# Optimization experiments

Measured on AMD Instinct MI355X. Metric: run time of the kernel, lower is better.

The kernel has to match this reference:

```python
import jax, jax.numpy as jnp
import numpy as np
from jax import lax

N_NODES = 100000
N_EDGES = 600000  # even: edges stored as consecutive reverse pairs
NODE_F = 64
EDGE_F = 16
EDGE_H = 128
NODE_H = 128
NUM_STEPS = 6


def setup_inputs() -> dict:
    key = jax.random.key(0)
    ks = jax.random.split(key, 16)
    # paired reverse edges: edge 2k is (src,dst), edge 2k+1 is (dst,src)
    src = jax.random.randint(ks[0], (N_EDGES // 2,), 0, N_NODES, dtype=jnp.int32)
    dst = jax.random.randint(ks[1], (N_EDGES // 2,), 0, N_NODES, dtype=jnp.int32)
    from_nodes = jnp.stack([src, dst], axis=1).reshape(-1)
    to_nodes = jnp.stack([dst, src], axis=1).reshape(-1)
    edges = jnp.stack([from_nodes, to_nodes], axis=0)
    return {
        "node_features": jax.random.normal(ks[2], (N_NODES, NODE_F), jnp.float32),
        "edge_features": jax.random.normal(ks[3], (N_EDGES, EDGE_F), jnp.float32),
        "edge_hiddens": jnp.zeros((N_EDGES, EDGE_H), jnp.float32),
        "edges": edges,
        "W1_w": jax.random.normal(ks[4], (NODE_F, EDGE_H), jnp.float32) / np.sqrt(NODE_F),
        "W1_b": jnp.zeros((EDGE_H,), jnp.float32),
        "W2_w": jax.random.normal(ks[5], (EDGE_F, EDGE_H), jnp.float32) / np.sqrt(EDGE_F),
        "W2_b": jnp.zeros((EDGE_H,), jnp.float32),
        "W3_w": jax.random.normal(ks[6], (EDGE_H, EDGE_H), jnp.float32) / np.sqrt(EDGE_H),
        "W3_b": jnp.zeros((EDGE_H,), jnp.float32),
        "U1_w": jax.random.normal(ks[7], (NODE_F, NODE_H), jnp.float32) / np.sqrt(NODE_F),
        "U1_b": jnp.zeros((NODE_H,), jnp.float32),
        "U2_w": jax.random.normal(ks[8], (EDGE_H, NODE_H), jnp.float32) / np.sqrt(EDGE_H),
        "U2_b": jnp.zeros((NODE_H,), jnp.float32),
    }


def reference(node_features, edge_features, edge_hiddens, edges,
              W1_w, W1_b, W2_w, W2_b, W3_w, W3_b, U1_w, U1_b, U2_w, U2_b):
    from_nodes = edges[0]
    to_nodes = edges[1]
    n_edges = edges.shape[1]
    # backlink of edge i is its reverse pair: even i -> i+1, odd i -> i-1
    idx = jnp.arange(n_edges)
    backlink = idx + ((idx + 1) % 2) * 2 - 1

    # loop-invariant terms
    W1_x_u = (node_features @ W1_w + W1_b)[from_nodes]     # [E, EH]
    W2_x_uv = edge_features @ W2_w + W2_b                  # [E, EH]

    def step(h, _):
        # sum edge hiddens by source node, gather back per-edge, drop backlink
        s = jax.ops.segment_sum(h, from_nodes, num_segments=N_NODES)  # [N, EH]
        wu = s[from_nodes] - h[backlink]                               # [E, EH]
        h_new = jax.nn.relu(W1_x_u + W2_x_uv + (wu @ W3_w + W3_b))
        return h_new, None

    edge_h, _ = lax.scan(step, edge_hiddens, None, length=NUM_STEPS)

    U1_x_u = node_features @ U1_w + U1_b                   # [N, NH]
    U2_vu = edge_h @ U2_w + U2_b                           # [E, NH]
    agg = jax.ops.segment_sum(U2_vu, to_nodes, num_segments=N_NODES)
    node_hiddens = jax.nn.relu(U1_x_u + agg)               # [N, NH]
    return node_hiddens
```

## Files before the change

### kernel.cpp

```cpp
#include <hip/hip_runtime.h>
#include <hip/hip_bf16.h>

#define N_NODES 100000
#define N_EDGES 600000
#define SCAN_BLOCKS ((N_NODES + 255) / 256)

typedef __bf16 bf16;
typedef __bf16 bf16x2 __attribute__((ext_vector_type(2)));
typedef __bf16 bf16x4 __attribute__((ext_vector_type(4)));
typedef __bf16 bf16x8 __attribute__((ext_vector_type(8)));
typedef float f32x4 __attribute__((ext_vector_type(4)));

__global__ void deg_hist(const int* __restrict__ from, int* __restrict__ deg, int E) {
    int e = blockIdx.x * blockDim.x + threadIdx.x;
    if (e < E) atomicAdd(&deg[from[e]], 1);
}

__global__ __launch_bounds__(256) void block_sums(
    const int* __restrict__ deg, int* __restrict__ bsum)
{
    __shared__ int s[256];
    int i = blockIdx.x * 256 + threadIdx.x;
    s[threadIdx.x] = (i < N_NODES) ? deg[i] : 0;
    __syncthreads();
    for (int st = 128; st > 0; st >>= 1) {
        if (threadIdx.x < st) s[threadIdx.x] += s[threadIdx.x + st];
        __syncthreads();
    }
    if (threadIdx.x == 0) bsum[blockIdx.x] = s[0];
}

__global__ __launch_bounds__(256) void scan_partials(
    const int* __restrict__ bsum, int* __restrict__ bpref, int* __restrict__ off)
{
    __shared__ int s[SCAN_BLOCKS];
    for (int i = threadIdx.x; i < SCAN_BLOCKS; i += 256) s[i] = bsum[i];
    __syncthreads();
    if (threadIdx.x == 0) {
        int run = 0;
        for (int i = 0; i < SCAN_BLOCKS; i++) { int t = s[i]; s[i] = run; run += t; }
        off[N_NODES] = run;
    }
    __syncthreads();
    for (int i = threadIdx.x; i < SCAN_BLOCKS; i += 256) bpref[i] = s[i];
}

__global__ __launch_bounds__(256) void block_scan(
    const int* __restrict__ deg, const int* __restrict__ bpref,
    int* __restrict__ off, int* __restrict__ cursor)
{
    __shared__ int s[256];
    int i = blockIdx.x * 256 + threadIdx.x;
    int v = (i < N_NODES) ? deg[i] : 0;
    s[threadIdx.x] = v;
    __syncthreads();
    for (int st = 1; st < 256; st <<= 1) {
        int x = (threadIdx.x >= st) ? s[threadIdx.x - st] : 0;
        __syncthreads();
        s[threadIdx.x] += x;
        __syncthreads();
    }
    if (i < N_NODES) {
        int o = bpref[blockIdx.x] + s[threadIdx.x] - v;
        off[i] = o;
        cursor[i] = o;
    }
}

__global__ void scatter_csr(const int* __restrict__ from, int* __restrict__ cursor,
                            int* __restrict__ se, int* __restrict__ rank, int E) {
    int e = blockIdx.x * blockDim.x + threadIdx.x;
    if (e < E) {
        int p = atomicAdd(&cursor[from[e]], 1);
        se[p] = e;
        rank[e] = p;
    }
}

__global__ void make_maps(const int* __restrict__ se, const int* __restrict__ from,
                          const int* __restrict__ rank,
                          int* __restrict__ fromP, int* __restrict__ backP, int E) {
    int i = blockIdx.x * blockDim.x + threadIdx.x;
    if (i < E) {
        int e = se[i];
        fromP[i] = from[e];
        backP[i] = rank[e ^ 1];
    }
}

__global__ __launch_bounds__(256) void node_gemm(
    const float* __restrict__ A, const float* __restrict__ B,
    const float* __restrict__ bias, float* __restrict__ C, int M)
{
    __shared__ float As[16][65];
    __shared__ float Bs[16][128];
    int row0 = blockIdx.x * 64;
    int tid = threadIdx.x;
    int tx = tid & 15, ty = tid >> 4;
    float acc[4][8];
    #pragma unroll
    for (int i = 0; i < 4; i++)
        #pragma unroll
        for (int j = 0; j < 8; j++) acc[i][j] = 0.f;

    for (int kk = 0; kk < 64; kk += 16) {
        int m  = tid >> 2;
        int k4 = (tid & 3) * 4;
        float4 v = make_float4(0.f, 0.f, 0.f, 0.f);
        if (row0 + m < M)
            v = *(const float4*)(A + (size_t)(row0 + m) * 64 + kk + k4);
        As[k4 + 0][m] = v.x; As[k4 + 1][m] = v.y;
        As[k4 + 2][m] = v.z; As[k4 + 3][m] = v.w;
        #pragma unroll
        for (int t = 0; t < 2; t++) {
            int id = tid + t * 256;
            int k = id >> 5, n4 = (id & 31) * 4;
            *(float4*)(&Bs[k][n4]) = *(const float4*)(B + (size_t)(kk + k) * 128 + n4);
        }
        __syncthreads();
        #pragma unroll
        for (int k = 0; k < 16; k++) {
            float a[4], b[8];
            #pragma unroll
            for (int i = 0; i < 4; i++) a[i] = As[k][ty * 4 + i];
            #pragma unroll
            for (int j = 0; j < 8; j++) b[j] = Bs[k][tx + j * 16];
            #pragma unroll
            for (int i = 0; i < 4; i++)
                #pragma unroll
                for (int j = 0; j < 8; j++) acc[i][j] += a[i] * b[j];
        }
        __syncthreads();
    }
    #pragma unroll
    for (int i = 0; i < 4; i++) {
        int r = row0 + ty * 4 + i;
        if (r < M) {
            #pragma unroll
            for (int j = 0; j < 8; j++) {
                int c = tx + j * 16;
                C[(size_t)r * 128 + c] = acc[i][j] + bias[c];
            }
        }
    }
}

__global__ __launch_bounds__(256) void base_sorted(
    const float* __restrict__ nodeW1, const int* __restrict__ fromP,
    const int* __restrict__ se, const float* __restrict__ ef,
    const float* __restrict__ W2, const float* __restrict__ W2b,
    const float* __restrict__ W3b, bf16* __restrict__ baseP)
{
    int tid = threadIdx.x;
    int c0 = (tid & 31) * 4;
    int sub = tid >> 5;
    float4 w[16];
    #pragma unroll
    for (int k = 0; k < 16; k++) w[k] = *(const float4*)(W2 + k * 128 + c0);
    float4 bias;
    {
        float4 a = *(const float4*)(W2b + c0);
        float4 b = *(const float4*)(W3b + c0);
        bias = make_float4(a.x + b.x, a.y + b.y, a.z + b.z, a.w + b.w);
    }
    #pragma unroll 1
    for (int it = 0; it < 64; ++it) {
        int i = blockIdx.x * 512 + it * 8 + sub;
        if (i >= N_EDGES) break;
        const float* efr = ef + (size_t)se[i] * 16;
        float4 nv = *(const float4*)(nodeW1 + (size_t)fromP[i] * 128 + c0);
        float4 acc = make_float4(bias.x + nv.x, bias.y + nv.y,
                                 bias.z + nv.z, bias.w + nv.w);
        #pragma unroll
        for (int k = 0; k < 16; k++) {
            float s = efr[k];
            acc.x += s * w[k].x; acc.y += s * w[k].y;
            acc.z += s * w[k].z; acc.w += s * w[k].w;
        }
        bf16x4 o;
        o[0] = (bf16)acc.x; o[1] = (bf16)acc.y; o[2] = (bf16)acc.z; o[3] = (bf16)acc.w;
        *(bf16x4*)(baseP + (size_t)i * 128 + c0) = o;
    }
}

__global__ __launch_bounds__(256) void prep_weights(
    const float* __restrict__ W3, const float* __restrict__ U2,
    bf16* __restrict__ W3T, bf16* __restrict__ U2T)
{
    int i = blockIdx.x * 256 + threadIdx.x;
    if (i < 128 * 128) {
        int k = i >> 7, n = i & 127;
        W3T[n * 128 + k] = (bf16)W3[k * 128 + n];
        U2T[n * 128 + k] = (bf16)U2[k * 128 + n];
    }
}

__global__ __launch_bounds__(256) void edge_mfma_v7(
    const bf16* __restrict__ baseP, const bf16* __restrict__ gin,
    const bf16* __restrict__ S, const int* __restrict__ fromP,
    const int* __restrict__ backP, const bf16* __restrict__ BT,
    bf16* __restrict__ gout, bf16* __restrict__ goutB,
    int fused, int writeG)
{
    __shared__ bf16 Bsw[128 * 128];
    int tid = threadIdx.x;

    #pragma unroll
    for (int t = 0; t < 8; t++) {
        int c = tid + t * 256;
        int cmr = c & 15;
        int cq  = (c >> 4) & 3;
        int ckt = (c >> 6) & 3;
        int cn  = c >> 8;
        int brow = cn * 16 + cmr;
        int bcol = ckt * 32 + cq * 8;
        *(bf16x8*)&Bsw[(size_t)c * 8] =
            *(const bf16x8*)(BT + (size_t)brow * 128 + bcol);
    }
    __syncthreads();

    int wave = tid >> 6, lane = tid & 63;
    int quad = lane >> 4, mr = lane & 15;

    #pragma unroll 1
    for (int it = 0; it < 4; ++it) {
        int i0 = blockIdx.x * 256 + wave * 64 + it * 16;
        if (i0 >= N_EDGES) break;
        int i = i0 + mr;

        bf16x8 afr[4];
        if (!fused) {
            #pragma unroll
            for (int kt = 0; kt < 4; kt++) {
                bf16x8 bb = *(const bf16x8*)(baseP + (size_t)i * 128 + kt * 32 + quad * 8);
                #pragma unroll
                for (int j = 0; j < 8; j++)
                    afr[kt][j] = (bf16)fmaxf((float)bb[j], 0.f);
            }
        } else {
            const bf16* sr = S   + (size_t)fromP[i] * 128;
            const bf16* gr = gin + (size_t)i * 128;
            #pragma unroll
            for (int kt = 0; kt < 4; kt++) {
                int c = kt * 32 + quad * 8;
                bf16x8 bb = *(const bf16x8*)(baseP + (size_t)i * 128 + c);
                bf16x8 gg = *(const bf16x8*)(gr + c);
                bf16x8 ss = *(const bf16x8*)(sr + c);
                #pragma unroll
                for (int j = 0; j < 8; j++) {
                    float v = (float)bb[j] + (float)ss[j] - (float)gg[j];
                    afr[kt][j] = (bf16)fmaxf(v, 0.f);
                }
            }
        }

        f32x4 acc[8];
        #pragma unroll
        for (int n = 0; n < 8; n++) acc[n] = (f32x4){0.f, 0.f, 0.f, 0.f};
        #pragma unroll
        for (int kt = 0; kt < 4; kt++) {
            #pragma unroll
            for (int n = 0; n < 8; n++) {
                bf16x8 b = *(const bf16x8*)&Bsw[(size_t)(((n * 4 + kt) * 64) + lane) * 8];
                acc[n] = __builtin_amdgcn_mfma_f32_16x16x32_bf16(afr[kt], b, acc[n], 0, 0, 0);
            }
        }

        int rbase4 = i0 + quad * 4;
        int4 br4 = *(const int4*)(backP + rbase4);
        int brows[4] = {br4.x, br4.y, br4.z, br4.w};

        #pragma unroll
        for (int np = 0; np < 4; np++) {
            int n0 = np * 2;
            #pragma unroll
            for (int reg = 0; reg < 4; reg++) {
                float v0 = acc[n0][reg], v1 = acc[n0 + 1][reg];
                float o0 = __shfl_xor(v0, 1);
                float o1 = __shfl_xor(v1, 1);
                bf16x2 pk;
                int colb;
                if ((mr & 1) == 0) {
                    pk[0] = (bf16)v0; pk[1] = (bf16)o0;
                    colb = n0 * 16 + mr;
                } else {
                    pk[0] = (bf16)o1; pk[1] = (bf16)v1;
                    colb = (n0 + 1) * 16 + (mr ^ 1);
                }
                if (writeG) {
                    int row = rbase4 + reg;
                    *(bf16x2*)(gout + (size_t)row * 128 + colb) = pk;
                }
                *(bf16x2*)(goutB + (size_t)brows[reg] * 128 + colb) = pk;
            }
        }
    }
}

__global__ __launch_bounds__(256) void segsum_stream(
    const bf16* __restrict__ g, const int* __restrict__ off, bf16* __restrict__ S)
{
    int n = blockIdx.x * 4 + (threadIdx.x >> 6);
    if (n >= N_NODES) return;
    int lane = threadIdx.x & 63;
    int o0 = off[n], o1 = off[n + 1];
    float a0 = 0.f, a1 = 0.f;
    for (int p = o0; p < o1; ++p) {
        bf16x2 v = *(const bf16x2*)(g + (size_t)p * 128 + lane * 2);
        a0 += (float)v[0];
        a1 += (float)v[1];
    }
    bf16x2 o; o[0] = (bf16)a0; o[1] = (bf16)a1;
    *(bf16x2*)(S + (size_t)n * 128 + lane * 2) = o;
}

__global__ __launch_bounds__(256) void final_out_stream(
    const bf16* __restrict__ X, const int* __restrict__ off,
    const float* __restrict__ U1x, const float* __restrict__ U2b,
    float* __restrict__ out)
{
    int n = blockIdx.x * 4 + (threadIdx.x >> 6);
    if (n >= N_NODES) return;
    int lane = threadIdx.x & 63;
    int o0 = off[n], o1 = off[n + 1];
    float a0 = 0.f, a1 = 0.f;
    for (int p = o0; p < o1; ++p) {
        bf16x2 v = *(const bf16x2*)(X + (size_t)p * 128 + lane * 2);
        a0 += (float)v[0];
        a1 += (float)v[1];
    }
    float d = (float)(o1 - o0);
    float2 u = *(const float2*)(U1x + (size_t)n * 128 + lane * 2);
    float2 b = *(const float2*)(U2b + lane * 2);
    float r0 = fmaxf(u.x + a0 + d * b.x, 0.f);
    float r1 = fmaxf(u.y + a1 + d * b.y, 0.f);
    *(float2*)(out + (size_t)n * 128 + lane * 2) = make_float2(r0, r1);
}

extern "C" void kernel_launch(void* const* d_in, const int* in_sizes, int n_in,
                              void* d_out, int out_size, void* d_ws, size_t ws_size,
                              hipStream_t stream) {
    const float* nf  = (const float*)d_in[0];
    const float* ef  = (const float*)d_in[1];
    const int* edges = (const int*)d_in[3];
    const int* from  = edges;
    const float* W1w = (const float*)d_in[4];
    const float* W1b = (const float*)d_in[5];
    const float* W2w = (const float*)d_in[6];
    const float* W2b = (const float*)d_in[7];
    const float* W3w = (const float*)d_in[8];
    const float* W3b = (const float*)d_in[9];
    const float* U1w = (const float*)d_in[10];
    const float* U1b = (const float*)d_in[11];
    const float* U2w = (const float*)d_in[12];
    const float* U2b = (const float*)d_in[13];
    float* out = (float*)d_out;

    const size_t NODE_MAT = (size_t)N_NODES * 128;
    const size_t EDGE_MAT = (size_t)N_EDGES * 128;
    char* w = (char*)d_ws;
    float* nodeW1 = (float*)w; w += NODE_MAT * 4;
    bf16*  S      = (bf16*)w;  w += NODE_MAT * 2;
    bf16*  baseP  = (bf16*)w;  w += EDGE_MAT * 2;
    bf16*  G      = (bf16*)w;  w += EDGE_MAT * 2;
    bf16*  GB0    = (bf16*)w;  w += EDGE_MAT * 2;
    bf16*  GB1    = (bf16*)w;  w += EDGE_MAT * 2;
    bf16*  W3T    = (bf16*)w;  w += 128 * 128 * 2;
    bf16*  U2T    = (bf16*)w;  w += 128 * 128 * 2;
    int*   deg    = (int*)w;   w += (size_t)N_NODES * 4;
    int*   off    = (int*)w;   w += (size_t)(N_NODES + 1) * 4;
    int*   cursor = (int*)w;   w += (size_t)N_NODES * 4;
    int*   bsum   = (int*)w;   w += (size_t)SCAN_BLOCKS * 4;
    int*   bpref  = (int*)w;   w += (size_t)SCAN_BLOCKS * 4;
    int*   se     = (int*)w;   w += (size_t)N_EDGES * 4;
    int*   rank   = (int*)w;   w += (size_t)N_EDGES * 4;
    int*   fromP  = (int*)w;   w += (size_t)N_EDGES * 4;
    int*   backP  = (int*)w;   w += (size_t)N_EDGES * 4;

    hipMemsetAsync(deg, 0, (size_t)N_NODES * 4, stream);
    deg_hist<<<(N_EDGES + 255) / 256, 256, 0, stream>>>(from, deg, N_EDGES);
    block_sums<<<SCAN_BLOCKS, 256, 0, stream>>>(deg, bsum);
    scan_partials<<<1, 256, 0, stream>>>(bsum, bpref, off);
    block_scan<<<SCAN_BLOCKS, 256, 0, stream>>>(deg, bpref, off, cursor);
    scatter_csr<<<(N_EDGES + 255) / 256, 256, 0, stream>>>(from, cursor, se, rank, N_EDGES);
    make_maps<<<(N_EDGES + 255) / 256, 256, 0, stream>>>(se, from, rank, fromP, backP, N_EDGES);

    prep_weights<<<(128 * 128 + 255) / 256, 256, 0, stream>>>(W3w, U2w, W3T, U2T);
    node_gemm<<<(N_NODES + 63) / 64, 256, 0, stream>>>(nf, W1w, W1b, nodeW1, N_NODES);
    base_sorted<<<(N_EDGES + 511) / 512, 256, 0, stream>>>(
        nodeW1, fromP, se, ef, W2w, W2b, W3b, baseP);

    const int EGRID = (N_EDGES + 255) / 256;
    const int SGRID = (N_NODES + 3) / 4;

    bf16* GBa = GB0;
    bf16* GBb = GB1;

    edge_mfma_v7<<<EGRID, 256, 0, stream>>>(
        baseP, GBa, S, fromP, backP, W3T, G, GBb, 0, 1);
    segsum_stream<<<SGRID, 256, 0, stream>>>(G, off, S);
    { bf16* t = GBa; GBa = GBb; GBb = t; }

    for (int it = 1; it < 5; ++it) {
        edge_mfma_v7<<<EGRID, 256, 0, stream>>>(
            baseP, GBa, S, fromP, backP, W3T, G, GBb, 1, 1);
        segsum_stream<<<SGRID, 256, 0, stream>>>(G, off, S);
        { bf16* t = GBa; GBa = GBb; GBb = t; }
    }

    edge_mfma_v7<<<EGRID, 256, 0, stream>>>(
        baseP, GBa, S, fromP, backP, U2T, G, GBb, 1, 0);

    node_gemm<<<(N_NODES + 63) / 64, 256, 0, stream>>>(nf, U1w, U1b, nodeW1, N_NODES);
    final_out_stream<<<SGRID, 256, 0, stream>>>(GBb, off, nodeW1, U2b, out);
}
```

Measured before the change: 1.876 ms.

## Drop backlink scatter writes, gather backlink rows on read, prefetch next tile

The edge kernel no longer writes a second scattered copy of each output row at its backlink position. Instead it reads the backlink row of the previous output through a gather, and the final aggregation also gathers through backP. The edge kernel also software-prefetches the next 16-row tile's inputs into registers while computing the current tile. This halves edge-matrix writes per step and replaces scattered writes with scattered reads, at the cost of more live registers and extra index loads.

After: 1.896 ms. Within noise of the previous version (+1.1%).

```diff
diff --git a/kernel.cpp b/kernel.cpp
--- a/kernel.cpp
+++ b/kernel.cpp
@@ -195,12 +195,11 @@
     }
 }
 
-__global__ __launch_bounds__(256) void edge_mfma_v7(
+__global__ __launch_bounds__(256) void edge_mfma_v8(
     const bf16* __restrict__ baseP, const bf16* __restrict__ gin,
     const bf16* __restrict__ S, const int* __restrict__ fromP,
     const int* __restrict__ backP, const bf16* __restrict__ BT,
-    bf16* __restrict__ gout, bf16* __restrict__ goutB,
-    int fused, int writeG)
+    bf16* __restrict__ gout, int fused)
 {
     __shared__ bf16 Bsw[128 * 128];
     int tid = threadIdx.x;
@@ -221,37 +220,58 @@
 
     int wave = tid >> 6, lane = tid & 63;
     int quad = lane >> 4, mr = lane & 15;
+    int ibase = blockIdx.x * 256 + wave * 64;
+    if (ibase >= N_EDGES) return;
+
+    bf16x8 cbb[4], cgg[4], css[4];
+    {
+        int i0r = ibase + mr;
+        int frc = 0, bkc = 0;
+        if (fused) { frc = fromP[i0r]; bkc = backP[i0r]; }
+        #pragma unroll
+        for (int kt = 0; kt < 4; kt++) {
+            int c = kt * 32 + quad * 8;
+            cbb[kt] = *(const bf16x8*)(baseP + (size_t)i0r * 128 + c);
+            if (fused) {
+                cgg[kt] = *(const bf16x8*)(gin + (size_t)bkc * 128 + c);
+                css[kt] = *(const bf16x8*)(S   + (size_t)frc * 128 + c);
+            }
+        }
+    }
 
     #pragma unroll 1
     for (int it = 0; it < 4; ++it) {
-        int i0 = blockIdx.x * 256 + wave * 64 + it * 16;
-        if (i0 >= N_EDGES) break;
-        int i = i0 + mr;
+        bf16x8 nbb[4], ngg[4], nss[4];
+        if (it < 3) {
+            int i_n = ibase + (it + 1) * 16 + mr;
+            int frn = 0, bkn = 0;
+            if (fused) { frn = fromP[i_n]; bkn = backP[i_n]; }
+            #pragma unroll
+            for (int kt = 0; kt < 4; kt++) {
+                int c = kt * 32 + quad * 8;
+                nbb[kt] = *(const bf16x8*)(baseP + (size_t)i_n * 128 + c);
+                if (fused) {
+                    ngg[kt] = *(const bf16x8*)(gin + (size_t)bkn * 128 + c);
+                    nss[kt] = *(const bf16x8*)(S   + (size_t)frn * 128 + c);
+                }
+            }
+        }
 
         bf16x8 afr[4];
         if (!fused) {
             #pragma unroll
-            for (int kt = 0; kt < 4; kt++) {
-                bf16x8 bb = *(const bf16x8*)(baseP + (size_t)i * 128 + kt * 32 + quad * 8);
+            for (int kt = 0; kt < 4; kt++)
                 #pragma unroll
                 for (int j = 0; j < 8; j++)
-                    afr[kt][j] = (bf16)fmaxf((float)bb[j], 0.f);
-            }
+                    afr[kt][j] = (bf16)fmaxf((float)cbb[kt][j], 0.f);
         } else {
-            const bf16* sr = S   + (size_t)fromP[i] * 128;
-            const bf16* gr = gin + (size_t)i * 128;
-            #pragma unroll
-            for (int kt = 0; kt < 4; kt++) {
-                int c = kt * 32 + quad * 8;
-                bf16x8 bb = *(const bf16x8*)(baseP + (size_t)i * 128 + c);
-                bf16x8 gg = *(const bf16x8*)(gr + c);
-                bf16x8 ss = *(const bf16x8*)(sr + c);
+            #pragma unroll
+            for (int kt = 0; kt < 4; kt++)
                 #pragma unroll
                 for (int j = 0; j < 8; j++) {
-                    float v = (float)bb[j] + (float)ss[j] - (float)gg[j];
+                    float v = (float)cbb[kt][j] + (float)css[kt][j] - (float)cgg[kt][j];
                     afr[kt][j] = (bf16)fmaxf(v, 0.f);
                 }
-            }
         }
 
         f32x4 acc[8];
@@ -266,10 +286,7 @@
             }
         }
 
-        int rbase4 = i0 + quad * 4;
-        int4 br4 = *(const int4*)(backP + rbase4);
-        int brows[4] = {br4.x, br4.y, br4.z, br4.w};
-
+        int i0 = ibase + it * 16;
         #pragma unroll
         for (int np = 0; np < 4; np++) {
             int n0 = np * 2;
@@ -287,12 +304,16 @@
                     pk[0] = (bf16)o1; pk[1] = (bf16)v1;
                     colb = (n0 + 1) * 16 + (mr ^ 1);
                 }
-                if (writeG) {
-                    int row = rbase4 + reg;
-                    *(bf16x2*)(gout + (size_t)row * 128 + colb) = pk;
-                }
-                *(bf16x2*)(goutB + (size_t)brows[reg] * 128 + colb) = pk;
+                int row = i0 + quad * 4 + reg;
+                *(bf16x2*)(gout + (size_t)row * 128 + colb) = pk;
             }
+        }
+
+        #pragma unroll
+        for (int kt = 0; kt < 4; kt++) {
+            cbb[kt] = nbb[kt];
+            cgg[kt] = ngg[kt];
+            css[kt] = nss[kt];
         }
     }
 }
@@ -314,10 +335,10 @@
     *(bf16x2*)(S + (size_t)n * 128 + lane * 2) = o;
 }
 
-__global__ __launch_bounds__(256) void final_out_stream(
-    const bf16* __restrict__ X, const int* __restrict__ off,
-    const float* __restrict__ U1x, const float* __restrict__ U2b,
-    float* __restrict__ out)
+__global__ __launch_bounds__(256) void final_gather_out(
+    const bf16* __restrict__ gB, const int* __restrict__ off,
+    const int* __restrict__ backP, const float* __restrict__ U1x,
+    const float* __restrict__ U2b, float* __restrict__ out)
 {
     int n = blockIdx.x * 4 + (threadIdx.x >> 6);
     if (n >= N_NODES) return;
@@ -325,7 +346,8 @@
     int o0 = off[n], o1 = off[n + 1];
     float a0 = 0.f, a1 = 0.f;
     for (int p = o0; p < o1; ++p) {
-        bf16x2 v = *(const bf16x2*)(X + (size_t)p * 128 + lane * 2);
+        int e = backP[p];
+        bf16x2 v = *(const bf16x2*)(gB + (size_t)e * 128 + lane * 2);
         a0 += (float)v[0];
         a1 += (float)v[1];
     }
@@ -362,9 +384,8 @@
     float* nodeW1 = (float*)w; w += NODE_MAT * 4;
     bf16*  S      = (bf16*)w;  w += NODE_MAT * 2;
     bf16*  baseP  = (bf16*)w;  w += EDGE_MAT * 2;
-    bf16*  G      = (bf16*)w;  w += EDGE_MAT * 2;
-    bf16*  GB0    = (bf16*)w;  w += EDGE_MAT * 2;
-    bf16*  GB1    = (bf16*)w;  w += EDGE_MAT * 2;
+    bf16*  g0     = (bf16*)w;  w += EDGE_MAT * 2;
+    bf16*  g1     = (bf16*)w;  w += EDGE_MAT * 2;
     bf16*  W3T    = (bf16*)w;  w += 128 * 128 * 2;
     bf16*  U2T    = (bf16*)w;  w += 128 * 128 * 2;
     int*   deg    = (int*)w;   w += (size_t)N_NODES * 4;
@@ -392,25 +413,23 @@
 
     const int EGRID = (N_EDGES + 255) / 256;
     const int SGRID = (N_NODES + 3) / 4;
-
-    bf16* GBa = GB0;
-    bf16* GBb = GB1;
-
-    edge_mfma_v7<<<EGRID, 256, 0, stream>>>(
-        baseP, GBa, S, fromP, backP, W3T, G, GBb, 0, 1);
-    segsum_stream<<<SGRID, 256, 0, stream>>>(G, off, S);
-    { bf16* t = GBa; GBa = GBb; GBb = t; }
-
+    bf16* G[2] = {g0, g1};
+
+    edge_mfma_v8<<<EGRID, 256, 0, stream>>>(
+        baseP, G[0], S, fromP, backP, W3T, G[0], 0);
+    segsum_stream<<<SGRID, 256, 0, stream>>>(G[0], off, S);
+    int cur = 0;
     for (int it = 1; it < 5; ++it) {
-        edge_mfma_v7<<<EGRID, 256, 0, stream>>>(
-            baseP, GBa, S, fromP, backP, W3T, G, GBb, 1, 1);
-        segsum_stream<<<SGRID, 256, 0, stream>>>(G, off, S);
-        { bf16* t = GBa; GBa = GBb; GBb = t; }
-    }
-
-    edge_mfma_v7<<<EGRID, 256, 0, stream>>>(
-        baseP, GBa, S, fromP, backP, U2T, G, GBb, 1, 0);
+        edge_mfma_v8<<<EGRID, 256, 0, stream>>>(
+            baseP, G[cur], S, fromP, backP, W3T, G[cur ^ 1], 1);
+        cur ^= 1;
+        segsum_stream<<<SGRID, 256, 0, stream>>>(G[cur], off, S);
+    }
+    edge_mfma_v8<<<EGRID, 256, 0, stream>>>(
+        baseP, G[cur], S, fromP, backP, U2T, G[cur ^ 1], 1);
+    cur ^= 1;
 
     node_gemm<<<(N_NODES + 63) / 64, 256, 0, stream>>>(nf, U1w, U1b, nodeW1, N_NODES);
-    final_out_stream<<<SGRID, 256, 0, stream>>>(GBb, off, nodeW1, U2b, out);
-}
+    final_gather_out<<<SGRID, 256, 0, stream>>>(
+        G[cur], off, backP, nodeW1, U2b, out);
+}
```
